# Kernel optimization log

Hardware: AMD Instinct MI355X
Metric: run time of the kernel (lower is better)

Reference implementation:

```python
import jax, jax.numpy as jnp
import numpy as np

N, E = 50000, 400000
N_INP, H, D = 256, 4, 32
HID = H * D
TN, TE, L, N_OUT = 4, 6, 2, 16
SQRT_D = float(np.sqrt(D))


def setup_inputs() -> dict:
    key = jax.random.key(0)
    ks = jax.random.split(key, 16)
    s = 0.05
    return {
        "x": jax.random.normal(ks[0], (N, N_INP), jnp.float32),
        "adapt_W": jax.random.normal(ks[1], (TN, N_INP, HID), jnp.float32) * s,
        "adapt_b": jnp.zeros((TN, HID), jnp.float32),
        "Wk": jax.random.normal(ks[2], (L, TN, HID, HID), jnp.float32) * s,
        "Wq": jax.random.normal(ks[3], (L, TN, HID, HID), jnp.float32) * s,
        "Wv": jax.random.normal(ks[4], (L, TN, HID, HID), jnp.float32) * s,
        "pri": jnp.ones((L, H, TE), jnp.float32),
        "Wa": jax.random.normal(ks[5], (L, H, TE, D, D), jnp.float32) * s,
        "Wm": jax.random.normal(ks[6], (L, H, TE, D, D), jnp.float32) * s,
        "Wla": jax.random.normal(ks[7], (L, TN, HID, HID), jnp.float32) * s,
        "skip": jnp.ones((L, TN), jnp.float32),
        "gamma": jnp.ones((L, HID), jnp.float32),
        "beta": jnp.zeros((L, HID), jnp.float32),
        "out_W": jax.random.normal(ks[8], (HID, N_OUT), jnp.float32) * s,
        "out_b": jnp.zeros((N_OUT,), jnp.float32),
        "ntype": jax.random.randint(ks[9], (N,), 0, TN),
        "etype": jax.random.randint(ks[10], (E,), 0, TE),
        "src": jax.random.randint(ks[11], (E,), 0, N),
        "dst": jax.random.randint(ks[12], (E,), 0, N),
    }


def typed_linear(x, W, types):
    # out[i] = x[i] @ W[types[i]]  (TypedLinear / per-type nn.Linear loop)
    out = jnp.zeros((x.shape[0], W.shape[-1]), x.dtype)
    for t in range(W.shape[0]):
        out = jnp.where((types == t)[:, None], x @ W[t], out)
    return out


def hgt_layer(h, ntype, etype, src, dst, Wk, Wq, Wv, pri, Wa, Wm, Wla, skip, gamma, beta):
    k = typed_linear(h, Wk, ntype).reshape(N, H, D)
    q = typed_linear(h, Wq, ntype).reshape(N, H, D)
    v = typed_linear(h, Wv, ntype).reshape(N, H, D)
    k_e, q_e, v_e = k[src], q[dst], v[src]  # [E,H,D] gathers
    a = jnp.zeros((E, H), h.dtype)
    m = jnp.zeros((E, H, D), h.dtype)
    for t in range(TE):  # small fixed loop over edge types (relation matrices)
        sel = etype == t
        kw = jnp.einsum('ehd,hdo->eho', k_e, Wa[:, t])
        sc = (kw * q_e).sum(-1) * pri[:, t][None, :] / SQRT_D  # [E,H]
        a = jnp.where(sel[:, None], sc, a)
        mt = jnp.einsum('ehd,hdo->eho', v_e, Wm[:, t])
        m = jnp.where(sel[:, None, None], mt, m)
    # edge softmax over incoming edges of each destination node
    amax = jax.ops.segment_max(a, dst, num_segments=N)
    ex = jnp.exp(a - amax[dst])
    den = jax.ops.segment_sum(ex, dst, num_segments=N)
    attn = ex / den[dst]
    agg = jax.ops.segment_sum(m * attn[:, :, None], dst, num_segments=N).reshape(N, HID)
    ha = typed_linear(agg, Wla, ntype)
    alpha = jax.nn.sigmoid(skip)[ntype][:, None]
    out = ha * alpha + h * (1.0 - alpha)
    mu = out.mean(-1, keepdims=True)
    var = jnp.mean((out - mu) ** 2, -1, keepdims=True)
    return (out - mu) / jnp.sqrt(var + 1e-5) * gamma + beta


def forward(x, adapt_W, adapt_b, Wk, Wq, Wv, pri, Wa, Wm, Wla, skip, gamma, beta, out_W, out_b, ntype, etype, src, dst):
    # per-node-type adapt linear + exact GELU
    h = typed_linear(x, adapt_W, ntype) + adapt_b[ntype]
    h = jax.nn.gelu(h, approximate=False)
    for l in range(L):
        h = hgt_layer(h, ntype, etype, src, dst, Wk[l], Wq[l], Wv[l], pri[l], Wa[l], Wm[l], Wla[l], skip[l], gamma[l], beta[l])
    return h @ out_W + out_b


def reference(x, adapt_W, adapt_b, Wk, Wq, Wv, pri, Wa, Wm, Wla, skip, gamma, beta, out_W, out_b, ntype, etype, src, dst):
    return forward(x, adapt_W, adapt_b, Wk, Wq, Wv, pri, Wa, Wm, Wla, skip, gamma, beta, out_W, out_b, ntype, etype, src, dst)
```

## Files before the change

kernel.cpp:

```cpp
#include <hip/hip_runtime.h>
#include <hip/hip_bf16.h>
#include <math.h>

#define NN   50000
#define EE   400000
#define NINP 256
#define HH   4
#define DD   32
#define HIDD 128
#define TNN  4
#define TEE  6
#define LLL  2
#define NOUTT 16
#define NB   196


typedef __attribute__((ext_vector_type(8))) short bf16x8;
typedef __attribute__((ext_vector_type(4))) float f32x4;

__device__ __forceinline__ float bf_lo(unsigned u) { return __uint_as_float(u << 16); }
__device__ __forceinline__ float bf_hi(unsigned u) { return __uint_as_float(u & 0xFFFF0000u); }
__device__ __forceinline__ unsigned f2bf(float f) {
    unsigned u = __float_as_uint(f);
    u += 0x7FFFu + ((u >> 16) & 1u);
    return (u >> 16);
}

__global__ void k_init(int* __restrict__ deg, int* __restrict__ cur, int* __restrict__ ncnt,
                       int* __restrict__ ncur, int* __restrict__ nperm) {
    int i = blockIdx.x * 256 + threadIdx.x;
    if (i < NN) { deg[i] = 0; cur[i] = 0; }
    if (i < 16) { ncnt[i] = 0; ncur[i] = 0; }
    if (i < NN + 512) nperm[i] = -1;
}

__global__ void k_count_edges(const int* __restrict__ dst, int* __restrict__ deg) {
    int e = blockIdx.x * 256 + threadIdx.x;
    if (e < EE) atomicAdd(&deg[dst[e]], 1);
}
__global__ void k_count_types(const int* __restrict__ ntype, int* __restrict__ ncnt) {
    int n = blockIdx.x * 256 + threadIdx.x;
    int lane = threadIdx.x & 63;
    int t = (n < NN) ? ntype[n] : -1;
#pragma unroll
    for (int tt = 0; tt < TNN; tt++) {
        unsigned long long mask = __ballot(t == tt);
        if (mask && lane == (__ffsll((unsigned long long)mask) - 1))
            atomicAdd(&ncnt[tt], __popcll(mask));
    }
}
__global__ void k_scan1(const int* __restrict__ deg, int* __restrict__ bsum) {
    int i = blockIdx.x * 256 + threadIdx.x;
    int lane = threadIdx.x & 63, wv = threadIdx.x >> 6;
    __shared__ int ws[4];
    int x = (i < NN) ? deg[i] : 0;
#pragma unroll
    for (int off = 1; off < 64; off <<= 1) x += __shfl_xor(x, off);
    if (lane == 0) ws[wv] = x;
    __syncthreads();
    if (threadIdx.x == 0) bsum[blockIdx.x] = ws[0] + ws[1] + ws[2] + ws[3];
}
__global__ void k_scan2(const int* __restrict__ bsum, int* __restrict__ bpre,
                        const int* __restrict__ ncnt, int* __restrict__ meta) {
    __shared__ int ws[4];
    int tid = threadIdx.x, lane = tid & 63, wv = tid >> 6;
    int v = (tid < NB) ? bsum[tid] : 0;
    int x = v;
#pragma unroll
    for (int off = 1; off < 64; off <<= 1) {
        int y = __shfl_up(x, off);
        if (lane >= off) x += y;
    }
    if (lane == 63) ws[wv] = x;
    __syncthreads();
    if (tid == 0) { int a = 0; for (int w = 0; w < 4; w++) { int s = ws[w]; ws[w] = a; a += s; } }
    __syncthreads();
    if (tid < NB) bpre[tid] = x - v + ws[wv];
    if (tid == 0) {
        int acc = 0;
        meta[0] = 0;
        for (int t = 0; t < TNN; t++) { acc += ((ncnt[t] + 63) >> 6) << 6; meta[t + 1] = acc; }
    }
}
__global__ void k_scan3(const int* __restrict__ deg, const int* __restrict__ bpre,
                        int* __restrict__ offs) {
    int b = blockIdx.x;
    int tid = threadIdx.x, lane = tid & 63, wv = tid >> 6;
    int i = b * 256 + tid;
    __shared__ int ws[4];
    int v = (i < NN) ? deg[i] : 0;
    int x = v;
#pragma unroll
    for (int off = 1; off < 64; off <<= 1) {
        int y = __shfl_up(x, off);
        if (lane >= off) x += y;
    }
    if (lane == 63) ws[wv] = x;
    __syncthreads();
    if (tid == 0) { int a = 0; for (int w = 0; w < 4; w++) { int s = ws[w]; ws[w] = a; a += s; } }
    __syncthreads();
    if (i < NN) offs[i + 1] = x + ws[wv] + bpre[b];
    if (b == 0 && tid == 0) offs[0] = 0;
}
__global__ void k_scatter_edges(const int* __restrict__ dst, const int* __restrict__ src,
                                const int* __restrict__ etype, const int* __restrict__ offs,
                                int* __restrict__ cur, unsigned* __restrict__ se) {
    int e = blockIdx.x * 256 + threadIdx.x;
    if (e < EE) {
        int d = dst[e];
        int p = atomicAdd(&cur[d], 1);
        se[offs[d] + p] = ((unsigned)src[e] << 3) | (unsigned)etype[e];
    }
}
__global__ void k_scatter_nodes(const int* __restrict__ ntype, const int* __restrict__ meta,
                                int* __restrict__ ncur, int* __restrict__ nperm) {
    int n = blockIdx.x * 256 + threadIdx.x;
    int lane = threadIdx.x & 63;
    int t = (n < NN) ? ntype[n] : -1;
#pragma unroll
    for (int tt = 0; tt < TNN; tt++) {
        unsigned long long mask = __ballot(t == tt);
        if (t == tt) {
            int rank = __popcll(mask & ((1ull << lane) - 1ull));
            int leader = __ffsll((unsigned long long)mask) - 1;
            int b = 0;
            if (rank == 0) b = atomicAdd(&ncur[tt], __popcll(mask));
            b = __shfl(b, leader);
            nperm[meta[tt] + b + rank] = n;
        }
    }
}

__global__ void k_wt(const float* __restrict__ adapt_W, const float* __restrict__ Wk,
                     const float* __restrict__ Wla, unsigned short* __restrict__ adaptT,
                     unsigned short* __restrict__ Wf, unsigned short* __restrict__ WlaT) {
    __shared__ float Ts[64][68];
    int b = blockIdx.x, tid = threadIdx.x;
    const float* src;
    unsigned short* dst;
    int K, kt, nt;
    if (b < 32) {
        int t = b >> 3, tile = b & 7;
        K = 256; kt = tile >> 1; nt = tile & 1;
        src = adapt_W + (size_t)t * 256 * 128;
        dst = adaptT + (size_t)t * 128 * 256;
    } else if (b < 64) {
        int b2 = b - 32, l = b2 >> 4, r = b2 & 15, t = r >> 2, tile = r & 3;
        K = 128; kt = tile >> 1; nt = tile & 1;
        src = Wk + (size_t)(l * 4 + t) * 16384;
        dst = Wf + (size_t)(l * TNN + t) * 1664 * 128;
    } else {
        int b2 = b - 64, l = b2 >> 4, r = b2 & 15, t = r >> 2, tile = r & 3;
        K = 128; kt = tile >> 1; nt = tile & 1;
        src = Wla + (size_t)(l * 4 + t) * 16384;
        dst = WlaT + (size_t)(l * 4 + t) * 16384;
    }
    int k0 = kt * 64, n0 = nt * 64;
#pragma unroll
    for (int it = 0; it < 4; it++) {
        int idx = tid + it * 256;
        int row = idx >> 4, c4 = (idx & 15) * 4;
        *(float4*)(&Ts[row][c4]) = *(const float4*)(src + (size_t)(k0 + row) * 128 + n0 + c4);
    }
    __syncthreads();
#pragma unroll
    for (int it = 0; it < 2; it++) {
        int idx = tid + it * 256;
        int nn = idx >> 3, sg = (idx & 7) * 8;
        uint4 pk;
        pk.x = f2bf(Ts[sg + 0][nn]) | (f2bf(Ts[sg + 1][nn]) << 16);
        pk.y = f2bf(Ts[sg + 2][nn]) | (f2bf(Ts[sg + 3][nn]) << 16);
        pk.z = f2bf(Ts[sg + 4][nn]) | (f2bf(Ts[sg + 5][nn]) << 16);
        pk.w = f2bf(Ts[sg + 6][nn]) | (f2bf(Ts[sg + 7][nn]) << 16);
        *(uint4*)(dst + (size_t)(n0 + nn) * K + k0 + sg) = pk;
    }
}

__global__ void k_comb(const float* __restrict__ Wq, const float* __restrict__ Wa,
                       const float* __restrict__ Wv, const float* __restrict__ Wm,
                       const float* __restrict__ pri, unsigned short* __restrict__ Wf) {
    __shared__ float Ls[128][36];
    __shared__ float Ss[32][36];
    __shared__ unsigned short Ot[32][136];
    int b = blockIdx.x, tid = threadIdx.x;
    int mode = b / 192;
    int rem = b % 192;
    int l = rem / 96;
    int rem2 = rem % 96;
    int t = rem2 / 24;
    int ht = rem2 % 24;
    int hh = ht / 6, te = ht % 6;
    const float* L = (mode == 0 ? Wq : Wv) + ((size_t)(l * TNN + t)) * 16384;
    const float* S = (mode == 0 ? Wa : Wm) + ((size_t)((l * HH + hh) * TEE + te)) * 1024;
    float ps = (mode == 0) ? pri[(l * HH + hh) * TEE + te] * 0.17677669529663687f : 1.0f;
#pragma unroll
    for (int it = 0; it < 4; it++) {
        int idx = tid + it * 256;
        int kk = idx >> 3, c4 = (idx & 7) * 4;
        *(float4*)(&Ls[kk][c4]) = *(const float4*)(L + (size_t)kk * 128 + hh * 32 + c4);
    }
    {
        int r = tid >> 3, c4 = (tid & 7) * 4;
        *(float4*)(&Ss[r][c4]) = *(const float4*)(S + r * 32 + c4);
    }
    __syncthreads();
    int k = tid >> 1, half = tid & 1;
#pragma unroll
    for (int jj = 0; jj < 16; jj++) {
        int j = half * 16 + jj;
        float s = 0.f;
        if (mode == 0) {
#pragma unroll
            for (int o = 0; o < 32; o++) s += Ls[k][o] * Ss[j][o];
        } else {
#pragma unroll
            for (int d = 0; d < 32; d++) s += Ls[k][d] * Ss[d][j];
        }
        Ot[j][k] = (unsigned short)f2bf(s * ps);
    }
    __syncthreads();
    unsigned short* dst = Wf + ((size_t)(l * TNN + t) * 1664 + (mode == 0 ? 128 : 896)) * 128;
#pragma unroll
    for (int it = 0; it < 2; it++) {
        int idx = tid + it * 256;
        int j = idx >> 4, sg = (idx & 15) * 8;
        uint4 pk = *(const uint4*)(&Ot[j][sg]);
        int jg = (hh * 6 + te) * 32 + j;
        *(uint4*)(dst + (size_t)jg * 128 + sg) = pk;
    }
}

template <int K, int NCB, int EPI, int OMODE, int AF32>
__launch_bounds__(256) __global__
void k_gemm(const void* __restrict__ Av, const unsigned short* __restrict__ WT,
            const float* __restrict__ bias, float* __restrict__ Yf,
            unsigned short* __restrict__ Yb, const int* __restrict__ nperm,
            const int* __restrict__ meta) {
    __shared__ __align__(16) char smem[52224];
    unsigned short* Ab = (unsigned short*)smem;
    unsigned short* Bs = (unsigned short*)(smem + 17408);
    float* Cb = (float*)(smem + 17408);
    const int WIDTH = NCB * 128;
    int row0 = blockIdx.x * 64;
    if (row0 >= meta[4]) return;
    int t = 0;
    while (t < 3 && row0 >= meta[t + 1]) t++;
    const unsigned short* WTt = WT + (size_t)t * WIDTH * K;
    int tid = threadIdx.x;
    int lane = tid & 63, w = tid >> 6;
    int m = lane & 15, q = lane >> 4;

#pragma unroll 1
    for (int cb = 0; cb < NCB; cb++) {
        f32x4 acc[4][2];
#pragma unroll
        for (int rt = 0; rt < 4; rt++)
#pragma unroll
            for (int ct = 0; ct < 2; ct++) acc[rt][ct] = (f32x4){0.f, 0.f, 0.f, 0.f};
#pragma unroll
        for (int kc = 0; kc < K / 128; kc++) {
            __syncthreads();
            if (AF32) {
                const float* A = (const float*)Av;
#pragma unroll
                for (int it = 0; it < 8; it++) {
                    int idx = tid + it * 256;
                    int r = idx >> 5, c4 = (idx & 31) * 4;
                    int node = nperm[row0 + r];
                    float4 v = make_float4(0.f, 0.f, 0.f, 0.f);
                    if (node >= 0)
                        v = *(const float4*)(A + (size_t)node * K + kc * 128 + c4);
                    uint2 pk;
                    pk.x = f2bf(v.x) | (f2bf(v.y) << 16);
                    pk.y = f2bf(v.z) | (f2bf(v.w) << 16);
                    *(uint2*)(Ab + r * 136 + c4) = pk;
                }
            }
#pragma unroll
            for (int it = 0; it < 8; it++) {
                int idx = tid + it * 256;
                int n = idx >> 4, sg = idx & 15;
                *(uint4*)(Bs + n * 136 + sg * 8) =
                    *(const uint4*)(WTt + (size_t)(cb * 128 + n) * K + kc * 128 + sg * 8);
            }
            __syncthreads();
#pragma unroll
            for (int k0 = 0; k0 < 128; k0 += 32) {
                bf16x8 b0 = *(const bf16x8*)(Bs + (w * 32 + m) * 136 + k0 + q * 8);
                bf16x8 b1 = *(const bf16x8*)(Bs + (w * 32 + 16 + m) * 136 + k0 + q * 8);
#pragma unroll
                for (int rt = 0; rt < 4; rt++) {
                    bf16x8 a = *(const bf16x8*)(Ab + (rt * 16 + m) * 136 + k0 + q * 8);
                    acc[rt][0] = __builtin_amdgcn_mfma_f32_16x16x32_bf16(a, b0, acc[rt][0], 0, 0, 0);
                    acc[rt][1] = __builtin_amdgcn_mfma_f32_16x16x32_bf16(a, b1, acc[rt][1], 0, 0, 0);
                }
            }
        }
#pragma unroll 1
        for (int hf = 0; hf < 2; hf++) {
            __syncthreads();
            if ((w >> 1) == hf) {
#pragma unroll
                for (int rt = 0; rt < 4; rt++)
#pragma unroll
                    for (int ct = 0; ct < 2; ct++)
#pragma unroll
                        for (int r = 0; r < 4; r++)
                            Cb[(rt * 16 + q * 4 + r) * 68 + (w & 1) * 32 + ct * 16 + m] =
                                acc[rt][ct][r];
            }
            __syncthreads();
#pragma unroll
            for (int it = 0; it < 4; it++) {
                int idx = tid + it * 256;
                int row = idx >> 4, c4 = (idx & 15) * 4;
                int node = nperm[row0 + row];
                if (node < 0) continue;
                float4 v = *(const float4*)(Cb + row * 68 + c4);
                if (EPI == 1) {
                    float4 bv = *(const float4*)(bias + t * 128 + hf * 64 + c4);
                    v.x += bv.x; v.y += bv.y; v.z += bv.z; v.w += bv.w;
                    const float is2 = 0.70710678118654752f;
                    v.x = 0.5f * v.x * (1.f + erff(v.x * is2));
                    v.y = 0.5f * v.y * (1.f + erff(v.y * is2));
                    v.z = 0.5f * v.z * (1.f + erff(v.z * is2));
                    v.w = 0.5f * v.w * (1.f + erff(v.w * is2));
                }
                int col = cb * 128 + hf * 64 + c4;
                if (OMODE == 0 || OMODE == 2)
                    *(float4*)(Yf + (size_t)node * WIDTH + col) = v;
                if (OMODE == 1 || OMODE == 2) {
                    uint2 pk;
                    pk.x = f2bf(v.x) | (f2bf(v.y) << 16);
                    pk.y = f2bf(v.z) | (f2bf(v.w) << 16);
                    *(uint2*)(Yb + (size_t)node * WIDTH + col) = pk;
                }
            }
        }
    }
}

template <int NCB, int EPI>
__launch_bounds__(256) __global__
void k_gemm_reg(const unsigned short* __restrict__ A, const unsigned short* __restrict__ WT,
                unsigned short* __restrict__ Yb, const int* __restrict__ nperm,
                const int* __restrict__ meta, const float* __restrict__ skipv,
                const float* __restrict__ gamma, const float* __restrict__ beta,
                float* __restrict__ hres, unsigned short* __restrict__ hbout) {
    __shared__ __align__(16) char smem[34816];
    unsigned short* Bs = (unsigned short*)smem;
    unsigned short* Cb16 = (unsigned short*)smem;
    float* Cbf = (float*)smem;
    const int WIDTH = NCB * 128;
    int row0 = blockIdx.x * 64;
    if (row0 >= meta[4]) return;
    int t = 0;
    while (t < 3 && row0 >= meta[t + 1]) t++;
    const unsigned short* WTt = WT + (size_t)t * WIDTH * 128;
    int tid = threadIdx.x;
    int lane = tid & 63, w = tid >> 6;
    int m = lane & 15, q = lane >> 4;

    bf16x8 a[4][4];
#pragma unroll
    for (int rt = 0; rt < 4; rt++) {
        int nd = nperm[row0 + rt * 16 + m];
#pragma unroll
        for (int kk = 0; kk < 4; kk++) {
            if (nd >= 0)
                a[rt][kk] = *(const bf16x8*)(A + (size_t)nd * 128 + kk * 32 + q * 8);
            else
                a[rt][kk] = (bf16x8){0, 0, 0, 0, 0, 0, 0, 0};
        }
    }

#pragma unroll 1
    for (int cb = 0; cb < NCB; cb++) {
        f32x4 acc[4][2];
#pragma unroll
        for (int rt = 0; rt < 4; rt++)
#pragma unroll
            for (int ct = 0; ct < 2; ct++) acc[rt][ct] = (f32x4){0.f, 0.f, 0.f, 0.f};
        __syncthreads();
#pragma unroll
        for (int it = 0; it < 8; it++) {
            int idx = tid + it * 256;
            int n = idx >> 4, sg = idx & 15;
            *(uint4*)(Bs + n * 136 + sg * 8) =
                *(const uint4*)(WTt + (size_t)(cb * 128 + n) * 128 + sg * 8);
        }
        __syncthreads();
#pragma unroll
        for (int kk = 0; kk < 4; kk++) {
            bf16x8 b0 = *(const bf16x8*)(Bs + (w * 32 + m) * 136 + kk * 32 + q * 8);
            bf16x8 b1 = *(const bf16x8*)(Bs + (w * 32 + 16 + m) * 136 + kk * 32 + q * 8);
#pragma unroll
            for (int rt = 0; rt < 4; rt++) {
                acc[rt][0] = __builtin_amdgcn_mfma_f32_16x16x32_bf16(a[rt][kk], b0, acc[rt][0], 0, 0, 0);
                acc[rt][1] = __builtin_amdgcn_mfma_f32_16x16x32_bf16(a[rt][kk], b1, acc[rt][1], 0, 0, 0);
            }
        }
        __syncthreads();
        if (EPI == 2) {
#pragma unroll
            for (int rt = 0; rt < 4; rt++)
#pragma unroll
                for (int ct = 0; ct < 2; ct++)
#pragma unroll
                    for (int r = 0; r < 4; r++)
                        Cbf[(rt * 16 + q * 4 + r) * 132 + w * 32 + ct * 16 + m] = acc[rt][ct][r];
            __syncthreads();
            float alpha = 1.0f / (1.0f + __expf(-skipv[t]));
            int off = lane * 2;
            float2 g2 = *(const float2*)(gamma + off);
            float2 b2 = *(const float2*)(beta + off);
#pragma unroll 1
            for (int it = 0; it < 16; it++) {
                int row = w * 16 + it;
                int node = nperm[row0 + row];
                if (node < 0) continue;
                float ax = Cbf[row * 132 + off];
                float ay = Cbf[row * 132 + off + 1];
                float2 h2 = *(const float2*)(hres + (size_t)node * 128 + off);
                float ox = ax * alpha + h2.x * (1.f - alpha);
                float oy = ay * alpha + h2.y * (1.f - alpha);
                float s = ox + oy;
#pragma unroll
                for (int mm = 1; mm < 64; mm <<= 1) s += __shfl_xor(s, mm);
                float mu = s * (1.0f / 128.0f);
                float dx = ox - mu, dy = oy - mu;
                float v2 = dx * dx + dy * dy;
#pragma unroll
                for (int mm = 1; mm < 64; mm <<= 1) v2 += __shfl_xor(v2, mm);
                float rs = rsqrtf(v2 * (1.0f / 128.0f) + 1e-5f);
                float vx = dx * rs * g2.x + b2.x;
                float vy = dy * rs * g2.y + b2.y;
                *(float2*)(hres + (size_t)node * 128 + off) = make_float2(vx, vy);
                *(unsigned*)(hbout + (size_t)node * 128 + off) = f2bf(vx) | (f2bf(vy) << 16);
            }
        } else {
#pragma unroll
            for (int rt = 0; rt < 4; rt++)
#pragma unroll
                for (int ct = 0; ct < 2; ct++)
#pragma unroll
                    for (int r = 0; r < 4; r++)
                        Cb16[(rt * 16 + q * 4 + r) * 136 + w * 32 + ct * 16 + m] =
                            (unsigned short)f2bf(acc[rt][ct][r]);
            __syncthreads();
#pragma unroll
            for (int it = 0; it < 4; it++) {
                int idx = tid + it * 256;
                int row = idx >> 4, sg = idx & 15;
                int node = nperm[row0 + row];
                if (node < 0) continue;
                *(uint4*)(Yb + (size_t)node * WIDTH + cb * 128 + sg * 8) =
                    *(const uint4*)(Cb16 + row * 136 + sg * 8);
            }
        }
    }
}

__global__ void k_edge(const unsigned short* __restrict__ kqv,
                       const int* __restrict__ offs, const unsigned* __restrict__ se,
                       unsigned short* __restrict__ aggb) {
    int lane = threadIdx.x & 63;
    int wid = blockIdx.x * (blockDim.x >> 6) + (threadIdx.x >> 6);
    int nw = gridDim.x * (blockDim.x >> 6);
    int h = lane >> 4;
    int i2 = (lane & 15) * 2;
    int hoff = h * 32 + i2;
    for (int n = wid; n < NN; n += nw) {
        int e0 = offs[n], e1 = offs[n + 1];
        float ax = 0.f, ay = 0.f, den = 0.f;
        const unsigned short* qrow = kqv + (size_t)n * 1664 + 128;
        int s[4], t[4];
#pragma unroll
        for (int u = 0; u < 4; u++) {
            s[u] = 0; t[u] = 0;
            if (e0 + u < e1) { unsigned p0 = se[e0 + u]; s[u] = p0 >> 3; t[u] = p0 & 7; }
        }
        int j = e0;
        while (j + 3 < e1) {
            unsigned ku[4], qu[4], vu[4];
#pragma unroll
            for (int u = 0; u < 4; u++) {
                int to = (h * 6 + t[u]) * 32 + i2;
                ku[u] = *(const unsigned*)(kqv + (size_t)s[u] * 1664 + hoff);
                qu[u] = *(const unsigned*)(qrow + to);
                vu[u] = *(const unsigned*)(kqv + (size_t)s[u] * 1664 + 896 + to);
            }
            int jn = j + 4;
#pragma unroll
            for (int u = 0; u < 4; u++)
                if (jn + u < e1) { unsigned p0 = se[jn + u]; s[u] = p0 >> 3; t[u] = p0 & 7; }
            float p[4];
#pragma unroll
            for (int u = 0; u < 4; u++)
                p[u] = bf_lo(ku[u]) * bf_lo(qu[u]) + bf_hi(ku[u]) * bf_hi(qu[u]);
#pragma unroll
            for (int mm = 1; mm < 16; mm <<= 1) {
#pragma unroll
                for (int u = 0; u < 4; u++) p[u] += __shfl_xor(p[u], mm);
            }
#pragma unroll
            for (int u = 0; u < 4; u++) {
                float ex = __expf(p[u]);
                den += ex;
                ax += ex * bf_lo(vu[u]);
                ay += ex * bf_hi(vu[u]);
            }
            j = jn;
        }
        for (int u = 0; j < e1; j++, u++) {
            int to = (h * 6 + t[u]) * 32 + i2;
            unsigned ku = *(const unsigned*)(kqv + (size_t)s[u] * 1664 + hoff);
            unsigned qu = *(const unsigned*)(qrow + to);
            unsigned vu = *(const unsigned*)(kqv + (size_t)s[u] * 1664 + 896 + to);
            float p0 = bf_lo(ku) * bf_lo(qu) + bf_hi(ku) * bf_hi(qu);
            p0 += __shfl_xor(p0, 1);
            p0 += __shfl_xor(p0, 2);
            p0 += __shfl_xor(p0, 4);
            p0 += __shfl_xor(p0, 8);
            float ex = __expf(p0);
            den += ex;
            ax += ex * bf_lo(vu);
            ay += ex * bf_hi(vu);
        }
        float r = (den > 0.f) ? (1.0f / den) : 0.f;
        unsigned pk = f2bf(ax * r) | (f2bf(ay * r) << 16);
        *(unsigned*)(aggb + (size_t)n * 128 + hoff) = pk;
    }
}

__global__ void k_out(const unsigned short* __restrict__ hb, const float* __restrict__ Wo,
                      const float* __restrict__ bo, float* __restrict__ out) {
    __shared__ float Ws[128 * 16];
    int tid = threadIdx.x;
#pragma unroll
    for (int it = 0; it < 2; it++) {
        int idx = (tid + it * 256) * 4;
        *(float4*)(&Ws[idx]) = *(const float4*)(Wo + idx);
    }
    __syncthreads();
    int nl = tid >> 4;
    int o = tid & 15;
    int n = blockIdx.x * 16 + nl;
    float acc = bo[o];
    const unsigned short* hr = hb + (size_t)n * 128;
#pragma unroll
    for (int kk = 0; kk < 128; kk += 8) {
        uint4 hv = *(const uint4*)(hr + kk);
        acc += bf_lo(hv.x) * Ws[(kk + 0) * 16 + o] + bf_hi(hv.x) * Ws[(kk + 1) * 16 + o] +
               bf_lo(hv.y) * Ws[(kk + 2) * 16 + o] + bf_hi(hv.y) * Ws[(kk + 3) * 16 + o] +
               bf_lo(hv.z) * Ws[(kk + 4) * 16 + o] + bf_hi(hv.z) * Ws[(kk + 5) * 16 + o] +
               bf_lo(hv.w) * Ws[(kk + 6) * 16 + o] + bf_hi(hv.w) * Ws[(kk + 7) * 16 + o];
    }
    out[(size_t)n * 16 + o] = acc;
}

extern "C" void kernel_launch(void* const* d_in, const int* in_sizes, int n_in,
                              void* d_out, int out_size, void* d_ws, size_t ws_size,
                              hipStream_t stream) {
    const float* x       = (const float*)d_in[0];
    const float* adapt_W = (const float*)d_in[1];
    const float* adapt_b = (const float*)d_in[2];
    const float* Wk      = (const float*)d_in[3];
    const float* Wq      = (const float*)d_in[4];
    const float* Wv      = (const float*)d_in[5];
    const float* pri     = (const float*)d_in[6];
    const float* Wa      = (const float*)d_in[7];
    const float* Wm      = (const float*)d_in[8];
    const float* Wla     = (const float*)d_in[9];
    const float* skip    = (const float*)d_in[10];
    const float* gamma   = (const float*)d_in[11];
    const float* beta    = (const float*)d_in[12];
    const float* out_W   = (const float*)d_in[13];
    const float* out_b   = (const float*)d_in[14];
    const int* ntype     = (const int*)d_in[15];
    const int* etype     = (const int*)d_in[16];
    const int* src       = (const int*)d_in[17];
    const int* dst       = (const int*)d_in[18];
    float* out = (float*)d_out;

    char* p = (char*)d_ws;
    auto al = [](size_t v) { return (v + 255) & ~(size_t)255; };
    float* h  = (float*)p;          p += al((size_t)NN * 128 * 4);
    unsigned short* hb   = (unsigned short*)p; p += al((size_t)NN * 128 * 2);
    unsigned short* aggb = (unsigned short*)p; p += al((size_t)NN * 128 * 2);
    unsigned short* kqvb = (unsigned short*)p; p += al((size_t)NN * 1664 * 2);
    unsigned short* adaptT = (unsigned short*)p; p += al((size_t)TNN * 128 * 256 * 2);
    unsigned short* WlaT   = (unsigned short*)p; p += al((size_t)LLL * TNN * 16384 * 2);
    unsigned short* Wf     = (unsigned short*)p; p += al((size_t)LLL * TNN * 1664 * 128 * 2);
    int* deg   = (int*)p; p += al((size_t)NN * 4);
    int* offs  = (int*)p; p += al((size_t)(NN + 1) * 4);
    int* cur   = (int*)p; p += al((size_t)NN * 4);
    unsigned* se = (unsigned*)p; p += al((size_t)EE * 4);
    int* nperm = (int*)p; p += al((size_t)(NN + 512) * 4);
    int* bsum  = (int*)p; p += al(256 * 4);
    int* bpre  = (int*)p; p += al(256 * 4);
    int* ncnt  = (int*)p; p += al(64);
    int* ncur  = (int*)p; p += al(64);
    int* meta  = (int*)p; p += al(64);

    k_init<<<(NN + 512 + 255) / 256, 256, 0, stream>>>(deg, cur, ncnt, ncur, nperm);
    k_count_edges<<<(EE + 255) / 256, 256, 0, stream>>>(dst, deg);
    k_count_types<<<(NN + 255) / 256, 256, 0, stream>>>(ntype, ncnt);
    k_scan1<<<NB, 256, 0, stream>>>(deg, bsum);
    k_scan2<<<1, 256, 0, stream>>>(bsum, bpre, ncnt, meta);
    k_scan3<<<NB, 256, 0, stream>>>(deg, bpre, offs);
    k_scatter_edges<<<(EE + 255) / 256, 256, 0, stream>>>(dst, src, etype, offs, cur, se);
    k_scatter_nodes<<<(NN + 255) / 256, 256, 0, stream>>>(ntype, meta, ncur, nperm);

    k_wt<<<96, 256, 0, stream>>>(adapt_W, Wk, Wla, adaptT, Wf, WlaT);
    k_comb<<<384, 256, 0, stream>>>(Wq, Wa, Wv, Wm, pri, Wf);

    const int TILES = NN / 64 + TNN + 1;

    k_gemm<256, 1, 1, 2, 1><<<TILES, 256, 0, stream>>>(
        x, adaptT, adapt_b, h, hb, nperm, meta);

    for (int l = 0; l < LLL; l++) {
        k_gemm_reg<13, 0><<<TILES, 256, 0, stream>>>(
            hb, Wf + (size_t)l * TNN * 1664 * 128, kqvb, nperm, meta,
            nullptr, nullptr, nullptr, nullptr, nullptr);

        k_edge<<<4096, 256, 0, stream>>>(kqvb, offs, se, aggb);

        k_gemm_reg<1, 2><<<TILES, 256, 0, stream>>>(
            aggb, WlaT + (size_t)l * TNN * 16384, nullptr, nperm, meta,
            skip + (size_t)l * TNN, gamma + (size_t)l * HIDD, beta + (size_t)l * HIDD,
            h, hb);
    }

    k_out<<<NN / 16, 256, 0, stream>>>(hb, out_W, out_b, out);
}
```

Before: 605.2 us.

## Load GEMM weight panels via direct global-to-LDS with XOR swizzle; split column blocks

Weight panels are now pre-swizzled (XOR on the k-column by row&7) when written by the transpose/combine kernels, so the register-A GEMM can stream each 128x128 bf16 panel straight into LDS with global_load_lds instead of staging through registers into a padded layout. Reads from LDS use the matching XOR index to avoid bank conflicts without padding, which also shrinks shared memory. The wide K/Q/V projection GEMM is also split two ways across column blocks, doubling the grid to improve occupancy, at the cost of loading the A tile twice.

```diff
diff --git a/kernel.cpp b/kernel.cpp
--- a/kernel.cpp
+++ b/kernel.cpp
@@ -26,6 +26,12 @@
     return (u >> 16);
 }
 
+__device__ __forceinline__ void gload_lds16(const unsigned short* g, unsigned short* l) {
+    __builtin_amdgcn_global_load_lds(
+        (__attribute__((address_space(1))) void*)(g),
+        (__attribute__((address_space(3))) void*)(l), 16, 0, 0);
+}
+
 __global__ void k_init(int* __restrict__ deg, int* __restrict__ cur, int* __restrict__ ncnt,
                        int* __restrict__ ncur, int* __restrict__ nperm) {
     int i = blockIdx.x * 256 + threadIdx.x;
@@ -138,20 +144,20 @@
     int b = blockIdx.x, tid = threadIdx.x;
     const float* src;
     unsigned short* dst;
-    int K, kt, nt;
+    int K, kt, nt, swz;
     if (b < 32) {
         int t = b >> 3, tile = b & 7;
-        K = 256; kt = tile >> 1; nt = tile & 1;
+        K = 256; kt = tile >> 1; nt = tile & 1; swz = 0;
         src = adapt_W + (size_t)t * 256 * 128;
         dst = adaptT + (size_t)t * 128 * 256;
     } else if (b < 64) {
         int b2 = b - 32, l = b2 >> 4, r = b2 & 15, t = r >> 2, tile = r & 3;
-        K = 128; kt = tile >> 1; nt = tile & 1;
+        K = 128; kt = tile >> 1; nt = tile & 1; swz = 1;
         src = Wk + (size_t)(l * 4 + t) * 16384;
         dst = Wf + (size_t)(l * TNN + t) * 1664 * 128;
     } else {
         int b2 = b - 64, l = b2 >> 4, r = b2 & 15, t = r >> 2, tile = r & 3;
-        K = 128; kt = tile >> 1; nt = tile & 1;
+        K = 128; kt = tile >> 1; nt = tile & 1; swz = 1;
         src = Wla + (size_t)(l * 4 + t) * 16384;
         dst = WlaT + (size_t)(l * 4 + t) * 16384;
     }
@@ -172,7 +178,9 @@
         pk.y = f2bf(Ts[sg + 2][nn]) | (f2bf(Ts[sg + 3][nn]) << 16);
         pk.z = f2bf(Ts[sg + 4][nn]) | (f2bf(Ts[sg + 5][nn]) << 16);
         pk.w = f2bf(Ts[sg + 6][nn]) | (f2bf(Ts[sg + 7][nn]) << 16);
-        *(uint4*)(dst + (size_t)(n0 + nn) * K + k0 + sg) = pk;
+        int col = k0 + sg;
+        if (swz) col ^= (nn & 7) << 3;
+        *(uint4*)(dst + (size_t)(n0 + nn) * K + col) = pk;
     }
 }
 
@@ -226,7 +234,7 @@
         int j = idx >> 4, sg = (idx & 15) * 8;
         uint4 pk = *(const uint4*)(&Ot[j][sg]);
         int jg = (hh * 6 + te) * 32 + j;
-        *(uint4*)(dst + (size_t)jg * 128 + sg) = pk;
+        *(uint4*)(dst + (size_t)jg * 128 + (sg ^ ((jg & 7) << 3))) = pk;
     }
 }
 
@@ -340,19 +348,22 @@
     }
 }
 
-template <int NCB, int EPI>
+template <int NCB, int EPI, int SPLIT>
 __launch_bounds__(256) __global__
 void k_gemm_reg(const unsigned short* __restrict__ A, const unsigned short* __restrict__ WT,
                 unsigned short* __restrict__ Yb, const int* __restrict__ nperm,
                 const int* __restrict__ meta, const float* __restrict__ skipv,
                 const float* __restrict__ gamma, const float* __restrict__ beta,
                 float* __restrict__ hres, unsigned short* __restrict__ hbout) {
-    __shared__ __align__(16) char smem[34816];
+    constexpr int SMEMB = (EPI == 2) ? 33792 : 32768;
+    __shared__ __align__(16) char smem[SMEMB];
     unsigned short* Bs = (unsigned short*)smem;
     unsigned short* Cb16 = (unsigned short*)smem;
     float* Cbf = (float*)smem;
     const int WIDTH = NCB * 128;
-    int row0 = blockIdx.x * 64;
+    int tile = blockIdx.x / SPLIT;
+    int par = blockIdx.x % SPLIT;
+    int row0 = tile * 64;
     if (row0 >= meta[4]) return;
     int t = 0;
     while (t < 3 && row0 >= meta[t + 1]) t++;
@@ -375,25 +386,27 @@
     }
 
 #pragma unroll 1
-    for (int cb = 0; cb < NCB; cb++) {
+    for (int cb = par; cb < NCB; cb += SPLIT) {
         f32x4 acc[4][2];
 #pragma unroll
         for (int rt = 0; rt < 4; rt++)
 #pragma unroll
             for (int ct = 0; ct < 2; ct++) acc[rt][ct] = (f32x4){0.f, 0.f, 0.f, 0.f};
         __syncthreads();
-#pragma unroll
-        for (int it = 0; it < 8; it++) {
-            int idx = tid + it * 256;
-            int n = idx >> 4, sg = idx & 15;
-            *(uint4*)(Bs + n * 136 + sg * 8) =
-                *(const uint4*)(WTt + (size_t)(cb * 128 + n) * 128 + sg * 8);
+        {
+            const unsigned short* pan = WTt + (size_t)cb * 128 * 128;
+#pragma unroll
+            for (int it = 0; it < 8; it++) {
+                int chunk = (it << 2) | w;
+                gload_lds16(pan + chunk * 512 + lane * 8, Bs + chunk * 512);
+            }
         }
         __syncthreads();
 #pragma unroll
         for (int kk = 0; kk < 4; kk++) {
-            bf16x8 b0 = *(const bf16x8*)(Bs + (w * 32 + m) * 136 + kk * 32 + q * 8);
-            bf16x8 b1 = *(const bf16x8*)(Bs + (w * 32 + 16 + m) * 136 + kk * 32 + q * 8);
+            int c = (kk * 32 + q * 8) ^ ((m & 7) << 3);
+            bf16x8 b0 = *(const bf16x8*)(Bs + (w * 32 + m) * 128 + c);
+            bf16x8 b1 = *(const bf16x8*)(Bs + (w * 32 + 16 + m) * 128 + c);
 #pragma unroll
             for (int rt = 0; rt < 4; rt++) {
                 acc[rt][0] = __builtin_amdgcn_mfma_f32_16x16x32_bf16(a[rt][kk], b0, acc[rt][0], 0, 0, 0);
@@ -621,13 +634,13 @@
         x, adaptT, adapt_b, h, hb, nperm, meta);
 
     for (int l = 0; l < LLL; l++) {
-        k_gemm_reg<13, 0><<<TILES, 256, 0, stream>>>(
+        k_gemm_reg<13, 0, 2><<<TILES * 2, 256, 0, stream>>>(
             hb, Wf + (size_t)l * TNN * 1664 * 128, kqvb, nperm, meta,
             nullptr, nullptr, nullptr, nullptr, nullptr);
 
         k_edge<<<4096, 256, 0, stream>>>(kqvb, offs, se, aggb);
 
-        k_gemm_reg<1, 2><<<TILES, 256, 0, stream>>>(
+        k_gemm_reg<1, 2, 1><<<TILES, 256, 0, stream>>>(
             aggb, WlaT + (size_t)l * TNN * 16384, nullptr, nperm, meta,
             skip + (size_t)l * TNN, gamma + (size_t)l * HIDD, beta + (size_t)l * HIDD,
             h, hb);
```

Result: no change. 597.8 us (-1.2%).
